# Optimization experiments

Hardware: AMD Instinct MI355X
Metric: run time of the kernel (lower is better)

The kernel has to match this reference:

```python
import jax, jax.numpy as jnp
import numpy as np

N_EMBD = 1024
N_HEAD = 16
HEAD_DIM = N_EMBD // N_HEAD


def setup_inputs() -> dict:
    key = jax.random.key(0)
    k1, k2, k3 = jax.random.split(key, 3)
    x = jax.random.normal(k1, (4, 2048, N_EMBD), dtype=jnp.float32)
    w_qkv = jax.random.normal(k2, (N_EMBD, 3 * N_EMBD), dtype=jnp.float32) * (N_EMBD ** -0.5)
    w_proj = jax.random.normal(k3, (N_EMBD, N_EMBD), dtype=jnp.float32) * (N_EMBD ** -0.5)
    return {"x": x, "w_qkv": w_qkv, "w_proj": w_proj}


def reference(x, w_qkv, w_proj):
    B, T, C = x.shape
    qkv = jnp.einsum('btc,cd->btd', x, w_qkv)  # [B,T,3C]
    q, k, v = jnp.split(qkv, 3, axis=-1)
    def heads(t):
        return t.reshape(B, T, N_HEAD, HEAD_DIM).transpose(0, 2, 1, 3)  # [B,H,T,D]
    q, k, v = heads(q), heads(k), heads(v)
    scale = 1.0 / jnp.sqrt(jnp.asarray(HEAD_DIM, dtype=x.dtype))
    att = jnp.einsum('bhqd,bhkd->bhqk', q, k) * scale  # [B,H,T,T]
    causal = jnp.tril(jnp.ones((T, T), dtype=bool))
    att = jnp.where(causal[None, None], att, jnp.asarray(-jnp.inf, dtype=att.dtype))
    att = jax.nn.softmax(att, axis=-1)
    out = jnp.einsum('bhqk,bhkd->bhqd', att, v)  # [B,H,T,D]
    out = out.transpose(0, 2, 1, 3).reshape(B, T, C)
    return jnp.einsum('btc,cd->btd', out, w_proj)
```

## Files before the change

kernel.cpp:

```cpp
#include <hip/hip_runtime.h>
#include <cstdint>
#include <cstddef>
#include <type_traits>

typedef float  f32x4   __attribute__((ext_vector_type(4)));
typedef __bf16 bf16x8  __attribute__((ext_vector_type(8)));
typedef short  short4_t __attribute__((ext_vector_type(4)));
typedef short  short8_t __attribute__((ext_vector_type(8)));

__device__ __forceinline__ short f2bf(float f) {
  return __builtin_bit_cast(short, (__bf16)f);
}

__device__ __forceinline__ void gl_lds16(const void* g, void* l) {
  __builtin_amdgcn_global_load_lds((const __attribute__((address_space(1))) void*)g,
                                   (__attribute__((address_space(3))) void*)l, 16, 0, 0);
}

__global__ void convert_bf16(const float* __restrict__ X, short* __restrict__ Xb) {
  int i = (blockIdx.x * 256 + threadIdx.x) * 4;
  f32x4 v = *(const f32x4*)&X[i];
  short4_t o;
#pragma unroll
  for (int j = 0; j < 4; j++) o[j] = f2bf(v[j]);
  *(short4_t*)&Xb[i] = o;
}

__global__ void transpose_bf16(const float* __restrict__ W, short* __restrict__ WT,
                               int K, int N) {
  __shared__ float tile[32][33];
  int tx = threadIdx.x & 31, ty = threadIdx.x >> 5;
  int n0 = blockIdx.x * 32, k0 = blockIdx.y * 32;
#pragma unroll
  for (int i = 0; i < 32; i += 8)
    tile[ty + i][tx] = W[(size_t)(k0 + ty + i) * N + n0 + tx];
  __syncthreads();
#pragma unroll
  for (int i = 0; i < 32; i += 8)
    WT[(size_t)(n0 + ty + i) * K + k0 + tx] = f2bf(tile[tx][ty + i]);
}

template <int MODE>
__global__ __launch_bounds__(256, 2) void gemm_bt(
    const short* __restrict__ A, const short* __restrict__ Bt,
    float* __restrict__ outf, short* __restrict__ Qo, short* __restrict__ Ko,
    short* __restrict__ Vo, int M, int N, int K) {
  __shared__ alignas(16) short As[128 * 32];
  __shared__ alignas(16) short Bs[128 * 32];
  const int tid = threadIdx.x;
  const int lane = tid & 63;
  const int g = lane & 15, q = lane >> 4;
  const int wave = tid >> 6;
  const int m0 = blockIdx.y * 128, n0 = blockIdx.x * 128;
  const int wm = (wave >> 1) * 64, wn = (wave & 1) * 64;

  const int srow = tid >> 2;
  const int scol = (tid & 3) * 8;
  const short* ap0 = A  + (size_t)(m0 + srow) * K + scol;
  const short* ap1 = A  + (size_t)(m0 + 64 + srow) * K + scol;
  const short* bp0 = Bt + (size_t)(n0 + srow) * K + scol;
  const short* bp1 = Bt + (size_t)(n0 + 64 + srow) * K + scol;
  short* la0 = &As[tid * 8];
  short* la1 = &As[(tid + 256) * 8];
  short* lb0 = &Bs[tid * 8];
  short* lb1 = &Bs[(tid + 256) * 8];

  f32x4 acc[4][4] = {};

  for (int k0 = 0; k0 < K; k0 += 32) {
    __syncthreads();
    gl_lds16(ap0 + k0, la0);
    gl_lds16(ap1 + k0, la1);
    gl_lds16(bp0 + k0, lb0);
    gl_lds16(bp1 + k0, lb1);
    __syncthreads();
    bf16x8 af[4], bfr[4];
#pragma unroll
    for (int mt = 0; mt < 4; mt++)
      af[mt] = *(const bf16x8*)&As[(wm + mt * 16 + g) * 32 + q * 8];
#pragma unroll
    for (int nt = 0; nt < 4; nt++)
      bfr[nt] = *(const bf16x8*)&Bs[(wn + nt * 16 + g) * 32 + q * 8];
#pragma unroll
    for (int mt = 0; mt < 4; mt++)
#pragma unroll
      for (int nt = 0; nt < 4; nt++)
        acc[mt][nt] = __builtin_amdgcn_mfma_f32_16x16x32_bf16(af[mt], bfr[nt],
                                                              acc[mt][nt], 0, 0, 0);
  }

  if (MODE == 0) {
#pragma unroll
    for (int mt = 0; mt < 4; mt++)
#pragma unroll
      for (int nt = 0; nt < 4; nt++) {
        int n = n0 + wn + nt * 16 + g;
        int mbase = m0 + wm + mt * 16 + q * 4;
#pragma unroll
        for (int r = 0; r < 4; r++)
          outf[(size_t)(mbase + r) * N + n] = acc[mt][nt][r];
      }
  } else {
#pragma unroll
    for (int nt = 0; nt < 4; nt++) {
      int n = n0 + wn + nt * 16 + g;
      int which = n >> 10;
      int c = n & 1023;
      int h = c >> 6, d = c & 63;
#pragma unroll
      for (int mt = 0; mt < 4; mt++) {
        int mbase = m0 + wm + mt * 16 + q * 4;
        int b = mbase >> 11, t = mbase & 2047;
        if (which == 2) {
          short4_t pv;
#pragma unroll
          for (int r = 0; r < 4; r++) pv[r] = f2bf(acc[mt][nt][r]);
          *(short4_t*)&Vo[((size_t)((b << 4) + h) * 64 + d) * 2048 + t] = pv;
        } else {
          short* dst = (which == 0) ? Qo : Ko;
#pragma unroll
          for (int r = 0; r < 4; r++)
            dst[((size_t)((b << 4) + h) * 2048 + (t + r)) * 64 + d] =
                f2bf(acc[mt][nt][r]);
        }
      }
    }
  }
}

__global__ __launch_bounds__(256, 2) void attn_fwd(
    const short* __restrict__ Qg, const short* __restrict__ Kg,
    const short* __restrict__ Vt, short* __restrict__ Og) {
  __shared__ alignas(16) short Ps[4][32 * 136];
  __shared__ alignas(16) short Ks[128 * 72];
  __shared__ alignas(16) short VTs[64 * 136];

  const int tid = threadIdx.x, lane = tid & 63, wave = tid >> 6;
  const int g = lane & 15, q = lane >> 4;
  const int bh = blockIdx.y;
  const size_t base = (size_t)bh * (2048 * 64);
  const int b = bh >> 4, h = bh & 15;
  const float cs = 0.18033688011f;

  short8_t kreg[4], vreg[4];
  auto loadKV = [&](int kt) {
    const short* Kp  = Kg + base + (size_t)kt * 128 * 64;
    const short* Vtp = Vt + base + (size_t)kt * 128;
#pragma unroll
    for (int i = 0; i < 4; i++) {
      int c = tid + i * 256;
      kreg[i] = *(const short8_t*)&Kp[(c >> 3) * 64 + (c & 7) * 8];
      vreg[i] = *(const short8_t*)&Vtp[(size_t)(c >> 4) * 2048 + (c & 15) * 8];
    }
  };
  auto storeKV = [&]() {
#pragma unroll
    for (int i = 0; i < 4; i++) {
      int c = tid + i * 256;
      *(short8_t*)&Ks[(c >> 3) * 72 + (c & 7) * 8] = kreg[i];
      *(short8_t*)&VTs[(c >> 4) * 136 + (c & 15) * 8] = vreg[i];
    }
  };

  for (int half = 0; half < 2; half++) {
    const int qt = (half == 0) ? (int)blockIdx.x : 15 - (int)blockIdx.x;

    __syncthreads();
    {
      const short* Qp = Qg + base + (size_t)qt * 128 * 64;
      short* Qs = &Ps[0][0];
#pragma unroll
      for (int i = 0; i < 4; i++) {
        int c = tid + i * 256;
        *(short8_t*)&Qs[(c >> 3) * 72 + (c & 7) * 8] =
            *(const short8_t*)&Qp[(c >> 3) * 64 + (c & 7) * 8];
      }
    }
    __syncthreads();
    bf16x8 bq[2][2];
#pragma unroll
    for (int nt = 0; nt < 2; nt++)
#pragma unroll
      for (int kk = 0; kk < 2; kk++) {
        bf16x8 v = *(const bf16x8*)&Ps[0][(wave * 32 + nt * 16 + g) * 72 + kk * 32 + q * 8];
#pragma unroll
        for (int j = 0; j < 8; j++) v[j] = (__bf16)((float)v[j] * cs);
        bq[nt][kk] = v;
      }

    f32x4 ot[4][2] = {};
    float m_run[2] = {-1e30f, -1e30f};
    float l_run[2] = {0.0f, 0.0f};

    auto compute = [&](auto diagc, int kt) {
      constexpr bool DIAG = decltype(diagc)::value;
      f32x4 st[8][2] = {};
#pragma unroll
      for (int kk = 0; kk < 2; kk++)
#pragma unroll
        for (int mt = 0; mt < 8; mt++) {
          bf16x8 ak = *(const bf16x8*)&Ks[(mt * 16 + g) * 72 + kk * 32 + q * 8];
#pragma unroll
          for (int nt = 0; nt < 2; nt++)
            st[mt][nt] = __builtin_amdgcn_mfma_f32_16x16x32_bf16(ak, bq[nt][kk],
                                                                 st[mt][nt], 0, 0, 0);
        }

#pragma unroll
      for (int nt = 0; nt < 2; nt++) {
        const int qloc = wave * 32 + nt * 16 + g;
        float tmax = -1e30f;
#pragma unroll
        for (int mt = 0; mt < 8; mt++)
#pragma unroll
          for (int r = 0; r < 4; r++) {
            if (DIAG) {
              if (mt * 16 + q * 4 + r > qloc) st[mt][nt][r] = -1e30f;
            }
            tmax = fmaxf(tmax, st[mt][nt][r]);
          }
        tmax = fmaxf(tmax, __shfl_xor(tmax, 16));
        tmax = fmaxf(tmax, __shfl_xor(tmax, 32));
        const float mnew = fmaxf(m_run[nt], tmax);
        const float alpha = __builtin_amdgcn_exp2f(m_run[nt] - mnew);
        float psum = 0.0f;
        short* Pw = &Ps[wave][0];
#pragma unroll
        for (int mt = 0; mt < 8; mt++) {
          short4_t pk;
#pragma unroll
          for (int r = 0; r < 4; r++) {
            float p = __builtin_amdgcn_exp2f(st[mt][nt][r] - mnew);
            psum += p;
            pk[r] = f2bf(p);
          }
          *(short4_t*)&Pw[(nt * 16 + g) * 136 + mt * 16 + q * 4] = pk;
        }
        psum += __shfl_xor(psum, 16);
        psum += __shfl_xor(psum, 32);
        l_run[nt] = l_run[nt] * alpha + psum;
        m_run[nt] = mnew;
#pragma unroll
        for (int mt = 0; mt < 4; mt++) {
          ot[mt][nt][0] *= alpha; ot[mt][nt][1] *= alpha;
          ot[mt][nt][2] *= alpha; ot[mt][nt][3] *= alpha;
        }
      }

#pragma unroll
      for (int kk = 0; kk < 4; kk++) {
        bf16x8 pb[2];
#pragma unroll
        for (int nt = 0; nt < 2; nt++)
          pb[nt] = *(const bf16x8*)&Ps[wave][(nt * 16 + g) * 136 + kk * 32 + q * 8];
#pragma unroll
        for (int mt = 0; mt < 4; mt++) {
          bf16x8 av = *(const bf16x8*)&VTs[(mt * 16 + g) * 136 + kk * 32 + q * 8];
#pragma unroll
          for (int nt = 0; nt < 2; nt++)
            ot[mt][nt] = __builtin_amdgcn_mfma_f32_16x16x32_bf16(av, pb[nt],
                                                                 ot[mt][nt], 0, 0, 0);
        }
      }
    };

    loadKV(0);
    for (int kt = 0; kt < qt; kt++) {
      __syncthreads();
      storeKV();
      loadKV(kt + 1);
      __syncthreads();
      compute(std::integral_constant<bool, false>{}, kt);
    }
    __syncthreads();
    storeKV();
    __syncthreads();
    compute(std::integral_constant<bool, true>{}, qt);

#pragma unroll
    for (int nt = 0; nt < 2; nt++) {
      const float inv = 1.0f / l_run[nt];
      const int qrow = qt * 128 + wave * 32 + nt * 16 + g;
      size_t obase = ((size_t)b * 2048 + qrow) * 1024 + h * 64;
#pragma unroll
      for (int mt = 0; mt < 4; mt++) {
        short4_t ov;
#pragma unroll
        for (int r = 0; r < 4; r++) ov[r] = f2bf(ot[mt][nt][r] * inv);
        *(short4_t*)&Og[obase + mt * 16 + q * 4] = ov;
      }
    }
  }
}

extern "C" void kernel_launch(void* const* d_in, const int* in_sizes, int n_in,
                              void* d_out, int out_size, void* d_ws, size_t ws_size,
                              hipStream_t stream) {
  const float* x      = (const float*)d_in[0];
  const float* w_qkv  = (const float*)d_in[1];
  const float* w_proj = (const float*)d_in[2];
  float* out = (float*)d_out;

  char* ws = (char*)d_ws;
  short* xb     = (short*)(ws);
  short* wqkvT  = (short*)(ws + 16777216);
  short* wprojT = (short*)(ws + 23068672);
  short* Qb     = (short*)(ws + 25165824);
  short* Kb     = (short*)(ws + 41943040);
  short* Vtb    = (short*)(ws + 58720256);

  convert_bf16<<<8192, 256, 0, stream>>>(x, xb);
  {
    dim3 gq(96, 32); transpose_bf16<<<gq, 256, 0, stream>>>(w_qkv, wqkvT, 1024, 3072);
    dim3 gp(32, 32); transpose_bf16<<<gp, 256, 0, stream>>>(w_proj, wprojT, 1024, 1024);
  }
  {
    dim3 g(24, 64);
    gemm_bt<1><<<g, 256, 0, stream>>>(xb, wqkvT, nullptr, Qb, Kb, Vtb, 8192, 3072, 1024);
  }
  {
    dim3 g(8, 64);
    attn_fwd<<<g, 256, 0, stream>>>(Qb, Kb, Vtb, xb );
  }
  {
    dim3 g(8, 64);
    gemm_bt<0><<<g, 256, 0, stream>>>(xb, wprojT, out, nullptr, nullptr, nullptr,
                                      8192, 1024, 1024);
  }
}
```

Measured before the change: 259.7 us.

## Rewrite attention to 32x32 MFMA with register-resident P and direct global K/V loads

The attention kernel drops all shared-memory staging of Q, K, V and P. Each wave now loads its K and V fragments straight from global memory (relying on L1/L2 for reuse across waves) and uses 32x32x16 bf16 MFMAs. The probability matrix is kept in registers and rearranged into the B-operand layout with v_permlane32_swap instead of a round trip through LDS. The kernel also adds s_setprio around the MFMA sections and swaps grid dimensions so blocks that share a batch-head launch consecutively. This removes LDS traffic and block-wide barriers, but each wave now issues redundant global loads of K and V and gets no explicit prefetch overlap.

```diff
diff --git a/kernel.cpp b/kernel.cpp
--- a/kernel.cpp
+++ b/kernel.cpp
@@ -3,13 +3,21 @@
 #include <cstddef>
 #include <type_traits>
 
-typedef float  f32x4   __attribute__((ext_vector_type(4)));
-typedef __bf16 bf16x8  __attribute__((ext_vector_type(8)));
+typedef float  f32x4    __attribute__((ext_vector_type(4)));
+typedef float  f32x16   __attribute__((ext_vector_type(16)));
+typedef __bf16 bf16x8   __attribute__((ext_vector_type(8)));
 typedef short  short4_t __attribute__((ext_vector_type(4)));
 typedef short  short8_t __attribute__((ext_vector_type(8)));
+typedef unsigned int uint4_t __attribute__((ext_vector_type(4)));
 
 __device__ __forceinline__ short f2bf(float f) {
   return __builtin_bit_cast(short, (__bf16)f);
+}
+
+__device__ __forceinline__ unsigned pk2bf(float a, float b) {
+  unsigned lo = (unsigned short)__builtin_bit_cast(unsigned short, f2bf(a));
+  unsigned hi = (unsigned short)__builtin_bit_cast(unsigned short, f2bf(b));
+  return lo | (hi << 16);
 }
 
 __device__ __forceinline__ void gl_lds16(const void* g, void* l) {
@@ -131,165 +139,138 @@
 __global__ __launch_bounds__(256, 2) void attn_fwd(
     const short* __restrict__ Qg, const short* __restrict__ Kg,
     const short* __restrict__ Vt, short* __restrict__ Og) {
-  __shared__ alignas(16) short Ps[4][32 * 136];
-  __shared__ alignas(16) short Ks[128 * 72];
-  __shared__ alignas(16) short VTs[64 * 136];
-
   const int tid = threadIdx.x, lane = tid & 63, wave = tid >> 6;
-  const int g = lane & 15, q = lane >> 4;
-  const int bh = blockIdx.y;
+  const int c = lane & 31;
+  const int qh = lane >> 5;
+  const int bh = blockIdx.x;
+  const int b = bh >> 4, h = bh & 15;
   const size_t base = (size_t)bh * (2048 * 64);
-  const int b = bh >> 4, h = bh & 15;
   const float cs = 0.18033688011f;
 
-  short8_t kreg[4], vreg[4];
-  auto loadKV = [&](int kt) {
-    const short* Kp  = Kg + base + (size_t)kt * 128 * 64;
-    const short* Vtp = Vt + base + (size_t)kt * 128;
-#pragma unroll
-    for (int i = 0; i < 4; i++) {
-      int c = tid + i * 256;
-      kreg[i] = *(const short8_t*)&Kp[(c >> 3) * 64 + (c & 7) * 8];
-      vreg[i] = *(const short8_t*)&Vtp[(size_t)(c >> 4) * 2048 + (c & 15) * 8];
+  const short* Kp = Kg + base + (size_t)c * 64 + qh * 8;
+  const short* Vp = Vt + base + (size_t)c * 2048 + qh * 8;
+  const int q_rel = wave * 32 + c;
+
+  for (int half = 0; half < 2; half++) {
+    const int qt = (half == 0) ? (int)blockIdx.y : 15 - (int)blockIdx.y;
+    const int qrow = qt * 128 + wave * 32 + c;
+
+    bf16x8 bq[4];
+#pragma unroll
+    for (int ks = 0; ks < 4; ks++) {
+      bf16x8 v = *(const bf16x8*)&Qg[base + (size_t)qrow * 64 + ks * 16 + qh * 8];
+#pragma unroll
+      for (int j = 0; j < 8; j++) v[j] = (__bf16)((float)v[j] * cs);
+      bq[ks] = v;
     }
-  };
-  auto storeKV = [&]() {
-#pragma unroll
-    for (int i = 0; i < 4; i++) {
-      int c = tid + i * 256;
-      *(short8_t*)&Ks[(c >> 3) * 72 + (c & 7) * 8] = kreg[i];
-      *(short8_t*)&VTs[(c >> 4) * 136 + (c & 15) * 8] = vreg[i];
-    }
-  };
-
-  for (int half = 0; half < 2; half++) {
-    const int qt = (half == 0) ? (int)blockIdx.x : 15 - (int)blockIdx.x;
-
-    __syncthreads();
-    {
-      const short* Qp = Qg + base + (size_t)qt * 128 * 64;
-      short* Qs = &Ps[0][0];
-#pragma unroll
-      for (int i = 0; i < 4; i++) {
-        int c = tid + i * 256;
-        *(short8_t*)&Qs[(c >> 3) * 72 + (c & 7) * 8] =
-            *(const short8_t*)&Qp[(c >> 3) * 64 + (c & 7) * 8];
-      }
-    }
-    __syncthreads();
-    bf16x8 bq[2][2];
-#pragma unroll
-    for (int nt = 0; nt < 2; nt++)
-#pragma unroll
-      for (int kk = 0; kk < 2; kk++) {
-        bf16x8 v = *(const bf16x8*)&Ps[0][(wave * 32 + nt * 16 + g) * 72 + kk * 32 + q * 8];
-#pragma unroll
-        for (int j = 0; j < 8; j++) v[j] = (__bf16)((float)v[j] * cs);
-        bq[nt][kk] = v;
-      }
-
-    f32x4 ot[4][2] = {};
-    float m_run[2] = {-1e30f, -1e30f};
-    float l_run[2] = {0.0f, 0.0f};
-
-    auto compute = [&](auto diagc, int kt) {
+
+    f32x16 ot[2] = {};
+    float m_run = -1e30f, l_run = 0.0f;
+
+    auto step = [&](auto diagc, int kt) {
       constexpr bool DIAG = decltype(diagc)::value;
-      f32x4 st[8][2] = {};
-#pragma unroll
-      for (int kk = 0; kk < 2; kk++)
-#pragma unroll
-        for (int mt = 0; mt < 8; mt++) {
-          bf16x8 ak = *(const bf16x8*)&Ks[(mt * 16 + g) * 72 + kk * 32 + q * 8];
-#pragma unroll
-          for (int nt = 0; nt < 2; nt++)
-            st[mt][nt] = __builtin_amdgcn_mfma_f32_16x16x32_bf16(ak, bq[nt][kk],
-                                                                 st[mt][nt], 0, 0, 0);
+
+      bf16x8 af[4][4];
+      const short* Kt = Kp + kt * (128 * 64);
+#pragma unroll
+      for (int mt = 0; mt < 4; mt++)
+#pragma unroll
+        for (int ks = 0; ks < 4; ks++)
+          af[mt][ks] = *(const bf16x8*)&Kt[mt * (32 * 64) + ks * 16];
+
+      f32x16 st[4] = {};
+      __builtin_amdgcn_s_setprio(1);
+#pragma unroll
+      for (int mt = 0; mt < 4; mt++)
+#pragma unroll
+        for (int ks = 0; ks < 4; ks++)
+          st[mt] = __builtin_amdgcn_mfma_f32_32x32x16_bf16(af[mt][ks], bq[ks],
+                                                           st[mt], 0, 0, 0);
+      __builtin_amdgcn_s_setprio(0);
+
+      bf16x8 va[8][2];
+      const short* Vtt = Vp + kt * 128;
+#pragma unroll
+      for (int kb = 0; kb < 8; kb++)
+#pragma unroll
+        for (int mt = 0; mt < 2; mt++)
+          va[kb][mt] = *(const bf16x8*)&Vtt[mt * (32 * 2048) + kb * 16];
+
+      float tm[4];
+#pragma unroll
+      for (int mt = 0; mt < 4; mt++) {
+        float t = -1e30f;
+#pragma unroll
+        for (int r = 0; r < 16; r++) {
+          if (DIAG) {
+            int krel = mt * 32 + (r & 3) + 8 * (r >> 2) + 4 * qh;
+            if (krel > q_rel) st[mt][r] = -1e30f;
+          }
+          t = fmaxf(t, st[mt][r]);
         }
-
-#pragma unroll
-      for (int nt = 0; nt < 2; nt++) {
-        const int qloc = wave * 32 + nt * 16 + g;
-        float tmax = -1e30f;
-#pragma unroll
-        for (int mt = 0; mt < 8; mt++)
-#pragma unroll
-          for (int r = 0; r < 4; r++) {
-            if (DIAG) {
-              if (mt * 16 + q * 4 + r > qloc) st[mt][nt][r] = -1e30f;
-            }
-            tmax = fmaxf(tmax, st[mt][nt][r]);
-          }
-        tmax = fmaxf(tmax, __shfl_xor(tmax, 16));
-        tmax = fmaxf(tmax, __shfl_xor(tmax, 32));
-        const float mnew = fmaxf(m_run[nt], tmax);
-        const float alpha = __builtin_amdgcn_exp2f(m_run[nt] - mnew);
-        float psum = 0.0f;
-        short* Pw = &Ps[wave][0];
-#pragma unroll
-        for (int mt = 0; mt < 8; mt++) {
-          short4_t pk;
-#pragma unroll
-          for (int r = 0; r < 4; r++) {
-            float p = __builtin_amdgcn_exp2f(st[mt][nt][r] - mnew);
-            psum += p;
-            pk[r] = f2bf(p);
-          }
-          *(short4_t*)&Pw[(nt * 16 + g) * 136 + mt * 16 + q * 4] = pk;
+        tm[mt] = t;
+      }
+      float tmax = fmaxf(fmaxf(tm[0], tm[1]), fmaxf(tm[2], tm[3]));
+      tmax = fmaxf(tmax, __shfl_xor(tmax, 32));
+      const float mnew = fmaxf(m_run, tmax);
+      const float alpha = __builtin_amdgcn_exp2f(m_run - mnew);
+      float ps[4];
+#pragma unroll
+      for (int mt = 0; mt < 4; mt++) {
+        float s = 0.0f;
+#pragma unroll
+        for (int r = 0; r < 16; r++) {
+          float p = __builtin_amdgcn_exp2f(st[mt][r] - mnew);
+          s += p;
+          st[mt][r] = p;
         }
-        psum += __shfl_xor(psum, 16);
-        psum += __shfl_xor(psum, 32);
-        l_run[nt] = l_run[nt] * alpha + psum;
-        m_run[nt] = mnew;
-#pragma unroll
-        for (int mt = 0; mt < 4; mt++) {
-          ot[mt][nt][0] *= alpha; ot[mt][nt][1] *= alpha;
-          ot[mt][nt][2] *= alpha; ot[mt][nt][3] *= alpha;
-        }
-      }
-
-#pragma unroll
-      for (int kk = 0; kk < 4; kk++) {
-        bf16x8 pb[2];
-#pragma unroll
-        for (int nt = 0; nt < 2; nt++)
-          pb[nt] = *(const bf16x8*)&Ps[wave][(nt * 16 + g) * 136 + kk * 32 + q * 8];
-#pragma unroll
-        for (int mt = 0; mt < 4; mt++) {
-          bf16x8 av = *(const bf16x8*)&VTs[(mt * 16 + g) * 136 + kk * 32 + q * 8];
-#pragma unroll
-          for (int nt = 0; nt < 2; nt++)
-            ot[mt][nt] = __builtin_amdgcn_mfma_f32_16x16x32_bf16(av, pb[nt],
-                                                                 ot[mt][nt], 0, 0, 0);
-        }
-      }
+        ps[mt] = s;
+      }
+      float psum = (ps[0] + ps[1]) + (ps[2] + ps[3]);
+      psum += __shfl_xor(psum, 32);
+      l_run = l_run * alpha + psum;
+      m_run = mnew;
+#pragma unroll
+      for (int mt = 0; mt < 2; mt++)
+#pragma unroll
+        for (int r = 0; r < 16; r++) ot[mt][r] *= alpha;
+
+      __builtin_amdgcn_s_setprio(1);
+#pragma unroll
+      for (int kb = 0; kb < 8; kb++) {
+        const int mt = kb >> 1, rb = (kb & 1) * 8;
+        unsigned x0 = pk2bf(st[mt][rb + 0], st[mt][rb + 1]);
+        unsigned x1 = pk2bf(st[mt][rb + 2], st[mt][rb + 3]);
+        unsigned y0 = pk2bf(st[mt][rb + 4], st[mt][rb + 5]);
+        unsigned y1 = pk2bf(st[mt][rb + 6], st[mt][rb + 7]);
+        asm("v_permlane32_swap_b32 %0, %1" : "+v"(x0), "+v"(y0));
+        asm("v_permlane32_swap_b32 %0, %1" : "+v"(x1), "+v"(y1));
+        uint4_t pw;
+        pw[0] = x0; pw[1] = x1; pw[2] = y0; pw[3] = y1;
+        bf16x8 pb = __builtin_bit_cast(bf16x8, pw);
+#pragma unroll
+        for (int mt2 = 0; mt2 < 2; mt2++)
+          ot[mt2] = __builtin_amdgcn_mfma_f32_32x32x16_bf16(va[kb][mt2], pb,
+                                                            ot[mt2], 0, 0, 0);
+      }
+      __builtin_amdgcn_s_setprio(0);
     };
 
-    loadKV(0);
-    for (int kt = 0; kt < qt; kt++) {
-      __syncthreads();
-      storeKV();
-      loadKV(kt + 1);
-      __syncthreads();
-      compute(std::integral_constant<bool, false>{}, kt);
-    }
-    __syncthreads();
-    storeKV();
-    __syncthreads();
-    compute(std::integral_constant<bool, true>{}, qt);
-
-#pragma unroll
-    for (int nt = 0; nt < 2; nt++) {
-      const float inv = 1.0f / l_run[nt];
-      const int qrow = qt * 128 + wave * 32 + nt * 16 + g;
-      size_t obase = ((size_t)b * 2048 + qrow) * 1024 + h * 64;
-#pragma unroll
-      for (int mt = 0; mt < 4; mt++) {
+    for (int kt = 0; kt < qt; kt++)
+      step(std::integral_constant<bool, false>{}, kt);
+    step(std::integral_constant<bool, true>{}, qt);
+
+    const float inv = 1.0f / l_run;
+    const size_t obase = ((size_t)b * 2048 + qrow) * 1024 + h * 64 + qh * 4;
+#pragma unroll
+    for (int mt = 0; mt < 2; mt++)
+#pragma unroll
+      for (int rr = 0; rr < 4; rr++) {
         short4_t ov;
 #pragma unroll
-        for (int r = 0; r < 4; r++) ov[r] = f2bf(ot[mt][nt][r] * inv);
-        *(short4_t*)&Og[obase + mt * 16 + q * 4] = ov;
-      }
-    }
+        for (int i = 0; i < 4; i++) ov[i] = f2bf(ot[mt][rr * 4 + i] * inv);
+        *(short4_t*)&Og[obase + mt * 32 + rr * 8] = ov;
+      }
   }
 }
 
@@ -319,7 +300,7 @@
     gemm_bt<1><<<g, 256, 0, stream>>>(xb, wqkvT, nullptr, Qb, Kb, Vtb, 8192, 3072, 1024);
   }
   {
-    dim3 g(8, 64);
+    dim3 g(64, 8);
     attn_fwd<<<g, 256, 0, stream>>>(Qb, Kb, Vtb, xb );
   }
   {
```

New measurement: 318.6 us. 22.7% more time.
